# Kernel tuning notes

Hardware: AMD Instinct MI355X
Metric: run time of the kernel (lower is better)

## Reference

```python
import jax, jax.numpy as jnp
import numpy as np

N, E, S = 20000, 160000, 3        # nodes, edges, message-passing steps
L, NODE_D, EDGE_D, OUT = 128, 12, 7, 3
LN_EPS = 1e-5


def _mlp(x, W0, b0, W1, b1, W2, b2):
    # Linear -> ReLU -> Linear -> ReLU -> Linear (widths: in->L->L->out)
    h = jax.nn.relu(x @ W0 + b0)
    h = jax.nn.relu(h @ W1 + b1)
    return h @ W2 + b2


def _ln(h, g, b):
    mu = jnp.mean(h, axis=-1, keepdims=True)
    var = jnp.mean((h - mu) ** 2, axis=-1, keepdims=True)
    return (h - mu) * jax.lax.rsqrt(var + LN_EPS) * g + b


def setup_inputs() -> dict:
    ks = iter(jax.random.split(jax.random.key(0), 64))
    w = lambda *s: jax.random.normal(next(ks), s, jnp.float32) * 0.05
    z = lambda *s: jnp.zeros(s, jnp.float32)
    o = lambda *s: jnp.ones(s, jnp.float32)
    inp = {
        'node_x': jax.random.normal(next(ks), (N, NODE_D), jnp.float32),
        'edge_x': jax.random.normal(next(ks), (E, EDGE_D), jnp.float32),
        'enc_n_W0': w(NODE_D, L), 'enc_n_b0': z(L), 'enc_n_W1': w(L, L), 'enc_n_b1': z(L),
        'enc_n_W2': w(L, L), 'enc_n_b2': z(L), 'enc_n_g': o(L), 'enc_n_be': z(L),
        'enc_e_W0': w(EDGE_D, L), 'enc_e_b0': z(L), 'enc_e_W1': w(L, L), 'enc_e_b1': z(L),
        'enc_e_W2': w(L, L), 'enc_e_b2': z(L), 'enc_e_g': o(L), 'enc_e_be': z(L),
        'gnb_e_W0': w(S, 3 * L, L), 'gnb_e_b0': z(S, L), 'gnb_e_W1': w(S, L, L), 'gnb_e_b1': z(S, L),
        'gnb_e_W2': w(S, L, L), 'gnb_e_b2': z(S, L), 'gnb_e_g': o(S, L), 'gnb_e_be': z(S, L),
        'gnb_n_W0': w(S, 2 * L, L), 'gnb_n_b0': z(S, L), 'gnb_n_W1': w(S, L, L), 'gnb_n_b1': z(S, L),
        'gnb_n_W2': w(S, L, L), 'gnb_n_b2': z(S, L), 'gnb_n_g': o(S, L), 'gnb_n_be': z(S, L),
        'dec_W0': w(L, L), 'dec_b0': z(L), 'dec_W1': w(L, L), 'dec_b1': z(L),
        'dec_W2': w(L, OUT), 'dec_b2': z(OUT),
        'senders': jax.random.randint(next(ks), (E,), 0, N, jnp.int32),
        'receivers': jax.random.randint(next(ks), (E,), 0, N, jnp.int32),
    }
    return inp


def reference(node_x, edge_x,
              enc_n_W0, enc_n_b0, enc_n_W1, enc_n_b1, enc_n_W2, enc_n_b2, enc_n_g, enc_n_be,
              enc_e_W0, enc_e_b0, enc_e_W1, enc_e_b1, enc_e_W2, enc_e_b2, enc_e_g, enc_e_be,
              gnb_e_W0, gnb_e_b0, gnb_e_W1, gnb_e_b1, gnb_e_W2, gnb_e_b2, gnb_e_g, gnb_e_be,
              gnb_n_W0, gnb_n_b0, gnb_n_W1, gnb_n_b1, gnb_n_W2, gnb_n_b2, gnb_n_g, gnb_n_be,
              dec_W0, dec_b0, dec_W1, dec_b1, dec_W2, dec_b2,
              senders, receivers):
    num_nodes = node_x.shape[0]
    # Encoder: MLP + LayerNorm on nodes and edges
    nf = _ln(_mlp(node_x, enc_n_W0, enc_n_b0, enc_n_W1, enc_n_b1, enc_n_W2, enc_n_b2), enc_n_g, enc_n_be)
    ef = _ln(_mlp(edge_x, enc_e_W0, enc_e_b0, enc_e_W1, enc_e_b1, enc_e_W2, enc_e_b2), enc_e_g, enc_e_be)

    def step(carry, p):
        nf, ef = carry
        (eW0, eb0, eW1, eb1, eW2, eb2, eg, ebe,
         nW0, nb0, nW1, nb1, nW2, nb2, ng, nbe) = p
        # gather sender/receiver node features -> concat with edge features -> edge MLP
        cat_e = jnp.concatenate([nf[senders], nf[receivers], ef], axis=-1)  # [E, 3L]
        new_ef = _ln(_mlp(cat_e, eW0, eb0, eW1, eb1, eW2, eb2), eg, ebe)
        # scatter-sum updated edge features to receiver nodes
        agg = jax.ops.segment_sum(new_ef, receivers, num_segments=num_nodes)  # [N, L]
        new_nf = _ln(_mlp(jnp.concatenate([nf, agg], axis=-1), nW0, nb0, nW1, nb1, nW2, nb2), ng, nbe)
        # residual connections on both nodes and edges
        return (nf + new_nf, ef + new_ef), None

    step_params = (gnb_e_W0, gnb_e_b0, gnb_e_W1, gnb_e_b1, gnb_e_W2, gnb_e_b2, gnb_e_g, gnb_e_be,
                   gnb_n_W0, gnb_n_b0, gnb_n_W1, gnb_n_b1, gnb_n_W2, gnb_n_b2, gnb_n_g, gnb_n_be)
    (nf, ef), _ = jax.lax.scan(step, (nf, ef), step_params)

    # Decoder: MLP without LayerNorm
    return _mlp(nf, dec_W0, dec_b0, dec_W1, dec_b1, dec_W2, dec_b2)
```

## Files before the change

### kernel.cpp

```cpp
#include <hip/hip_runtime.h>
#include <hip/hip_bf16.h>

#define NN 20000
#define EE 160000

typedef __attribute__((ext_vector_type(8))) short bf16x8;
typedef __attribute__((ext_vector_type(4))) float f32x4;

__device__ __forceinline__ unsigned short f2bf(float f) {
    unsigned int u = __float_as_uint(f);
    u += 0x7FFFu + ((u >> 16) & 1);
    return (unsigned short)(u >> 16);
}
__device__ __forceinline__ float bf2f(short s) {
    return __uint_as_float(((unsigned int)(unsigned short)s) << 16);
}
__device__ __forceinline__ bf16x8 pack8(float4 a, float4 b) {
    bf16x8 r;
    r[0] = (short)f2bf(a.x); r[1] = (short)f2bf(a.y);
    r[2] = (short)f2bf(a.z); r[3] = (short)f2bf(a.w);
    r[4] = (short)f2bf(b.x); r[5] = (short)f2bf(b.y);
    r[6] = (short)f2bf(b.z); r[7] = (short)f2bf(b.w);
    return r;
}
// ... 20 lines not shown

__device__ __forceinline__ void mfma_sweep64(f32x4 (&acc)[2][8], bf16x8 a0, bf16x8 a1,
                                             const short* sWb, int colOff, int lm)
{
#pragma unroll
    for (int ct = 0; ct < 8; ++ct) {
        bf16x8 b = *(const bf16x8*)(sWb + (ct * 16 + lm) * SW64 + colOff);
        acc[0][ct] = __builtin_amdgcn_mfma_f32_16x16x32_bf16(a0, b, acc[0][ct], 0, 0, 0);
        acc[1][ct] = __builtin_amdgcn_mfma_f32_16x16x32_bf16(a1, b, acc[1][ct], 0, 0, 0);
    }
}

__device__ __forceinline__ void mfma_sweepNS(f32x4 (&acc)[4], bf16x8 a,
                                             const short* sWb, int ch, int colOff, int lm)
{
#pragma unroll
    for (int i = 0; i < 4; ++i) {
        int ct = ch * 4 + i;
        bf16x8 b = *(const bf16x8*)(sWb + (ct * 16 + lm) * SW64 + colOff);
        acc[i] = __builtin_amdgcn_mfma_f32_16x16x32_bf16(a, b, acc[i], 0, 0, 0);
    }
}

template<int NT>
struct WStage { bf16x8 v[512 / NT]; };

template<int NT>
__device__ __forceinline__ void wload(WStage<NT>& ws, const short* __restrict__ Wt,
                                      int Kpad, int k0, int tid)
{
#pragma unroll
    for (int j = 0; j < 256 / NT; ++j) {
        int i = tid + j * NT;
        int r = i >> 1, h = i & 1;
        const short* src = Wt + (size_t)r * Kpad + k0 + h * 16;
        ws.v[2 * j]     = *(const bf16x8*)src;
        ws.v[2 * j + 1] = *(const bf16x8*)(src + 8);
    }
}
template<int NT>
__device__ __forceinline__ void wstore(const WStage<NT>& ws, short* __restrict__ sW, int tid)
{
#pragma unroll
    for (int j = 0; j < 256 / NT; ++j) {
        int i = tid + j * NT;
        int r = i >> 1, h = i & 1;
        short* dst = sW + r * SW_STRIDE + h * 16;
        *(bf16x8*)dst       = ws.v[2 * j];
        *(bf16x8*)(dst + 8) = ws.v[2 * j + 1];
    }
}

struct WStage64 { bf16x8 v[4]; };
__device__ __forceinline__ void wload64(WStage64& ws, const short* __restrict__ Wt,
                                        int Kpad, int k0, int tid)
{
#pragma unroll
    for (int j = 0; j < 4; ++j) {
        int i = tid + j * 256;
        int r = i >> 3, h = i & 7;
        ws.v[j] = *(const bf16x8*)(Wt + (size_t)r * Kpad + k0 + h * 8);
    }
}
__device__ __forceinline__ void wstore64(const WStage64& ws, short* __restrict__ sW, int tid)
{
#pragma unroll
    for (int j = 0; j < 4; ++j) {
        int i = tid + j * 256;
        int r = i >> 3, h = i & 7;
        *(bf16x8*)(sW + r * SW64 + h * 8) = ws.v[j];
    }
}

// ... 35 lines not shown
            sH[(g16 + lq * 4 + reg) * SH_STRIDE + ct * 16 + lm] = (short)f2bf(v);
        }
    }
}

__device__ __forceinline__ void park64(const f32x4 (&acc)[2][8], const float* __restrict__ bias,
                                       short* __restrict__ sH, int w32, int lm, int lq)
{
#pragma unroll
    for (int ct = 0; ct < 8; ++ct) {
        float bb = bias[ct * 16 + lm];
#pragma unroll
        for (int rt = 0; rt < 2; ++rt) {
            int rbase = w32 + rt * 16 + lq * 4;
#pragma unroll
            for (int reg = 0; reg < 4; ++reg) {
                float v = fmaxf(acc[rt][ct][reg] + bb, 0.f);
                sH[(rbase + reg) * SH64 + ct * 16 + lm] = (short)f2bf(v);
            }
        }
    }
}

struct Frag {
    bf16x8 a0, a1;
    float4 f0, f1, f2, f3;
    int isF;
};

template<int MODE>
__device__ __forceinline__ void load_frag(Frag& fr, int c,
    const short* __restrict__ nfb, const float* __restrict__ aggf,
    int r0m, int r1m, const short* sH, int w32, int lm, int lq)
{
    int kq = lq * 8;
    fr.isF = 0;
    if (MODE == 0) {
        fr.a0 = *(const bf16x8*)&sH[(w32 + lm) * SH_STRIDE + c * 32 + kq];
        fr.a1 = *(const bf16x8*)&sH[(w32 + 16 + lm) * SH_STRIDE + c * 32 + kq];
    } else if (MODE == 2) {
        int seg = c >> 2, kb = (c & 3) * 32 + kq;
        if (seg == 0) {
            fr.a0 = *(const bf16x8*)(nfb + (size_t)r0m * 128 + kb);
            fr.a1 = *(const bf16x8*)(nfb + (size_t)r1m * 128 + kb);
        } else {
            const float* p0 = aggf + (size_t)r0m * 128 + kb;
            const float* p1 = aggf + (size_t)r1m * 128 + kb;
            fr.f0 = *(const float4*)p0; fr.f1 = *(const float4*)(p0 + 4);
            fr.f2 = *(const float4*)p1; fr.f3 = *(const float4*)(p1 + 4);
            fr.isF = 1;
        }
    } else {
        int kb = c * 32 + kq;
        fr.a0 = *(const bf16x8*)(nfb + (size_t)r0m * 128 + kb);
        fr.a1 = *(const bf16x8*)(nfb + (size_t)r1m * 128 + kb);
    }
}

template<int MODE>
__device__ __forceinline__ void load_fragNS(Frag& fr, int c,
    const short* __restrict__ nfb, const float* __restrict__ aggf, int r0m, int lq)
{
    fr.isF = 0;
    if (MODE == 2 && c >= 2) {
        const float* p = aggf + (size_t)r0m * 128 + (c - 2) * 64 + lq * 8;
        fr.f0 = *(const float4*)p;        fr.f1 = *(const float4*)(p + 4);
        fr.f2 = *(const float4*)(p + 32); fr.f3 = *(const float4*)(p + 36);
        fr.isF = 1;
    } else {
        const short* p = nfb + (size_t)r0m * 128 + c * 64 + lq * 8;
        fr.a0 = *(const bf16x8*)p;
        fr.a1 = *(const bf16x8*)(p + 32);
    }
}

struct Frag64 { bf16x8 a[4]; };

__device__ __forceinline__ void load_frag64(Frag64& fr, int c,
    const short* __restrict__ nfb, const short* __restrict__ efHi,
    int iS0, int iS1, int iR0, int iR1, size_t eO0, size_t eO1, int lq)
{
    int kb = (c & 1) * 64 + lq * 8;
    int seg = c >> 1;
    const short *base0, *base1;
    if (seg == 0)      { base0 = nfb + (size_t)iS0 * 128; base1 = nfb + (size_t)iS1 * 128; }
    else if (seg == 1) { base0 = nfb + (size_t)iR0 * 128; base1 = nfb + (size_t)iR1 * 128; }
    else               { base0 = efHi + eO0;              base1 = efHi + eO1; }
// ... 143 lines not shown
            }
        }
        if (rcv != curRcv) {
            if (curRcv >= 0) {
#pragma unroll
                for (int ct = 0; ct < 8; ++ct)
                    atomicAdd(aggOut + (size_t)curRcv * 128 + ct * 16 + lm, run[ct]);
            }
            curRcv = rcv;
#pragma unroll
            for (int ct = 0; ct < 8; ++ct) run[ct] = o[ct];
        } else {
#pragma unroll
            for (int ct = 0; ct < 8; ++ct) run[ct] += o[ct];
        }
    }
    if (curRcv >= 0) {
#pragma unroll
        for (int ct = 0; ct < 8; ++ct)
            atomicAdd(aggOut + (size_t)curRcv * 128 + ct * 16 + lm, run[ct]);
    }
}

template<int NW, int MODE, int PAIR>
__global__ __launch_bounds__(NW * 64) void gnn_mlp(
    const short* __restrict__ Wt0,
    const short* __restrict__ Wt1, const short* __restrict__ Wt2,
    const float* __restrict__ b0, const float* __restrict__ b1, const float* __restrict__ b2,
    const float* __restrict__ g, const float* __restrict__ be,
    const float* __restrict__ A0f, int K0,
    const short* __restrict__ nfb,
    const float* __restrict__ aggf,
    const int* __restrict__ eList,
    float* __restrict__ outF, short* __restrict__ outB,
    float* __restrict__ aggOut,
    float* __restrict__ decOut,
    int M, int resid)
{
    constexpr int KP0 = (MODE == 2) ? 256 : (MODE == 3) ? 128 : 32;
    constexpr int nC0 = KP0 / 32;
    __shared__ short sH[NW * 32 * SH_STRIDE];
    __shared__ short sW[128 * SW_STRIDE];
    const int tid = threadIdx.x;
    const int lane = tid & 63;
    const int w = tid >> 6;
    const int lm = lane & 15;
    const int lq = lane >> 4;
    const int w32 = w * 32;
    const int m0 = blockIdx.x * (NW * 32);
    constexpr int NT = NW * 64;

    f32x4 acc[2][8];
    zero_acc(acc);

    if (MODE == 0) {
#pragma unroll
        for (int i = 0; i < 16; ++i) {
            int flat = lane + i * 64;
            int r = flat >> 5, k = flat & 31;
            int row = m0 + w32 + r;
            float v = 0.f;
            if (k < K0 && row < M) {
                int src = eList ? eList[row] : row;
                v = A0f[(size_t)src * K0 + k];
            }
            sH[(w32 + r) * SH_STRIDE + k] = (short)f2bf(v);
        }
    }
    const int r0m = min(m0 + w32 + lm, M - 1);
    const int r1m = min(m0 + w32 + 16 + lm, M - 1);

    {
        WStage<NT> ws, wsn;
        Frag cur, nx1, nx2;
        wload<NT>(ws, Wt0, KP0, 0, tid);
        load_frag<MODE>(cur, 0, nfb, aggf, r0m, r1m, sH, w32, lm, lq);
        if (nC0 > 1)
            load_frag<MODE>(nx1, 1, nfb, aggf, r0m, r1m, sH, w32, lm, lq);
#pragma unroll
        for (int c = 0; c < nC0; ++c) {
            if (c + 1 < nC0)
                wload<NT>(wsn, Wt0, KP0, (c + 1) * 32, tid);
            if (c + 2 < nC0)
                load_frag<MODE>(nx2, c + 2, nfb, aggf, r0m, r1m, sH, w32, lm, lq);
            bar_lgkm();
            wstore<NT>(ws, sW, tid);
            bar_lgkm();
            bf16x8 u0, u1;
            if (cur.isF) { u0 = pack8(cur.f0, cur.f1); u1 = pack8(cur.f2, cur.f3); }
            else         { u0 = cur.a0;               u1 = cur.a1; }
            mfma_sweep_lds(acc, u0, u1, sW, lm, lq);
            ws = wsn; cur = nx1; nx1 = nx2;
        }
    }
    bar_lgkm();
    park(acc, b0, sH, w32, lm, lq);

    zero_acc(acc);
    {
        WStage<NT> ws, wsn;
        wload<NT>(ws, Wt1, 128, 0, tid);
#pragma unroll
        for (int c = 0; c < 4; ++c) {
            if (c + 1 < 4) wload<NT>(wsn, Wt1, 128, (c + 1) * 32, tid);
            bf16x8 a0 = *(const bf16x8*)&sH[(w32 + lm) * SH_STRIDE + c * 32 + lq * 8];
            bf16x8 a1 = *(const bf16x8*)&sH[(w32 + 16 + lm) * SH_STRIDE + c * 32 + lq * 8];
            bar_lgkm();
            wstore<NT>(ws, sW, tid);
            bar_lgkm();
            mfma_sweep_lds(acc, a0, a1, sW, lm, lq);
            ws = wsn;
        }
    }
    bar_lgkm();
    park(acc, b1, sH, w32, lm, lq);

    zero_acc(acc);
    {
        WStage<NT> ws, wsn;
        wload<NT>(ws, Wt2, 128, 0, tid);
#pragma unroll
        for (int c = 0; c < 4; ++c) {
            if (c + 1 < 4) wload<NT>(wsn, Wt2, 128, (c + 1) * 32, tid);
            bf16x8 a0 = *(const bf16x8*)&sH[(w32 + lm) * SH_STRIDE + c * 32 + lq * 8];
            bf16x8 a1 = *(const bf16x8*)&sH[(w32 + 16 + lm) * SH_STRIDE + c * 32 + lq * 8];
            bar_lgkm();
            wstore<NT>(ws, sW, tid);
            bar_lgkm();
            mfma_sweep_lds(acc, a0, a1, sW, lm, lq);
            ws = wsn;
        }
    }

    float g_[8], be_[8], b2_[8];
#pragma unroll
    for (int ct = 0; ct < 8; ++ct) {
        g_[ct] = g[ct * 16 + lm]; be_[ct] = be[ct * 16 + lm]; b2_[ct] = b2[ct * 16 + lm];
    }
#pragma unroll
    for (int rt = 0; rt < 2; ++rt) {
#pragma unroll
        for (int reg = 0; reg < 4; ++reg) {
            int row = m0 + w32 + rt * 16 + lq * 4 + reg;
            float v[8];
            float s = 0.f;
#pragma unroll
            for (int ct = 0; ct < 8; ++ct) { v[ct] = acc[rt][ct][reg] + b2_[ct]; s += v[ct]; }
            s += __shfl_xor(s, 1); s += __shfl_xor(s, 2);
            s += __shfl_xor(s, 4); s += __shfl_xor(s, 8);
            float mu = s * (1.f / 128.f);
            float q = 0.f;
#pragma unroll
            for (int ct = 0; ct < 8; ++ct) { v[ct] -= mu; q += v[ct] * v[ct]; }
            q += __shfl_xor(q, 1); q += __shfl_xor(q, 2);
            q += __shfl_xor(q, 4); q += __shfl_xor(q, 8);
            float rs = rsqrtf(q * (1.f / 128.f) + 1e-5f);
            if (row < M) {
#pragma unroll
                for (int ct = 0; ct < 8; ++ct) {
                    float o = v[ct] * rs * g_[ct] + be_[ct];
                    size_t gi = (size_t)row * 128 + ct * 16 + lm;
                    if (PAIR) {
                        outB[gi] = (short)f2bf(o);
                    } else {
                        if (resid) {
                            float ns = outF[gi] + o;
                            outF[gi] = ns;
                            if (outB) outB[gi] = (short)f2bf(ns);
                        } else {
                            outF[gi] = o;
                            if (outB) outB[gi] = (short)f2bf(o);
                        }
                    }
                }
            }
        }
    }
}

template<int MODE>
__global__ __launch_bounds__(256) void gnn_mlpNS(
    const short* __restrict__ Wt0,
    const short* __restrict__ Wt1, const short* __restrict__ Wt2,
    const float* __restrict__ b0, const float* __restrict__ b1, const float* __restrict__ b2,
    const float* __restrict__ g, const float* __restrict__ be,
    const float* __restrict__ A0f, int K0,
    const short* __restrict__ nfb,
    const float* __restrict__ aggf,
    float* __restrict__ outF, short* __restrict__ outB,
    float* __restrict__ aggOut,
    float* __restrict__ decOut,
    int M, int resid)
{
    __shared__ short sH[32 * SH_STRIDE];
    __shared__ short sW[128 * SW64];
    __shared__ float sX[2][32];
    __shared__ float sY[2][32];
    const int tid = threadIdx.x;
    const int lane = tid & 63;
    const int w = tid >> 6;
    const int gidx = w >> 1;
    const int ch = w & 1;
    const int lm = lane & 15;
    const int lq = lane >> 4;
    const int g16 = gidx * 16;
    const int m0 = blockIdx.x * 32;
    const int r0m = min(m0 + g16 + lm, M - 1);

    f32x4 acc[4];
#pragma unroll
    for (int i = 0; i < 4; ++i) acc[i] = (f32x4)(0.f);

    if (MODE == 0) {
#pragma unroll
        for (int i = 0; i < 4; ++i) {
            int flat = tid + i * 256;
            int r = flat >> 5, k = flat & 31;
            int row = m0 + r;
            float v = (k < K0 && row < M) ? A0f[(size_t)row * K0 + k] : 0.f;
            sH[r * SH_STRIDE + k] = (short)f2bf(v);
        }
        {
            const short* src = Wt0 + (size_t)(tid >> 1) * 32 + (tid & 1) * 16;
            bf16x8 w0 = *(const bf16x8*)src;
            bf16x8 w1 = *(const bf16x8*)(src + 8);
            bar_lgkm();
            short* dst = sW + (tid >> 1) * SW64 + (tid & 1) * 16;
            *(bf16x8*)dst       = w0;
            *(bf16x8*)(dst + 8) = w1;
            bar_lgkm();
        }
        bf16x8 a0 = *(const bf16x8*)&sH[(g16 + lm) * SH_STRIDE + lq * 8];
        mfma_sweepNS(acc, a0, sW, ch, lq * 8, lm);
    } else {
        constexpr int KP0 = (MODE == 2) ? 256 : 128;
        constexpr int nC0 = KP0 / 64;
        WStage64 ws, wsn;
        Frag cur, nxt;
        wload64(ws, Wt0, KP0, 0, tid);
        load_fragNS<MODE>(cur, 0, nfb, aggf, r0m, lq);
#pragma unroll
        for (int c = 0; c < nC0; ++c) {
            if (c + 1 < nC0) {
                wload64(wsn, Wt0, KP0, (c + 1) * 64, tid);
                load_fragNS<MODE>(nxt, c + 1, nfb, aggf, r0m, lq);
            }
            bar_lgkm();
            wstore64(ws, sW, tid);
            bar_lgkm();
            bf16x8 u0, u1;
            if (cur.isF) { u0 = pack8(cur.f0, cur.f1); u1 = pack8(cur.f2, cur.f3); }
            else         { u0 = cur.a0;                u1 = cur.a1; }
            mfma_sweepNS(acc, u0, sW, ch, lq * 8, lm);
            mfma_sweepNS(acc, u1, sW, ch, 32 + lq * 8, lm);
            ws = wsn; cur = nxt;
        }
    }
    bar_lgkm();
    parkNS(acc, b0, sH, g16, ch, lm, lq);
    bar_lgkm();

    if (MODE == 2 && aggOut) {
#pragma unroll
        for (int i = 0; i < 4; ++i) {
            int idx = tid + i * 256;
            int r = idx >> 5, c4 = idx & 31;
            int row = m0 + r;
            if (row < M)
// ... 3 lines not shown

#pragma unroll
    for (int i = 0; i < 4; ++i) acc[i] = (f32x4)(0.f);
    {
        WStage64 ws, wsn;
        wload64(ws, Wt1, 128, 0, tid);
#pragma unroll
        for (int c = 0; c < 2; ++c) {
            if (c == 0) wload64(wsn, Wt1, 128, 64, tid);
            bf16x8 a0 = *(const bf16x8*)&sH[(g16 + lm) * SH_STRIDE + c * 64 + lq * 8];
            bf16x8 a1 = *(const bf16x8*)&sH[(g16 + lm) * SH_STRIDE + c * 64 + 32 + lq * 8];
            bar_lgkm();
            wstore64(ws, sW, tid);
            bar_lgkm();
            mfma_sweepNS(acc, a0, sW, ch, lq * 8, lm);
            mfma_sweepNS(acc, a1, sW, ch, 32 + lq * 8, lm);
            ws = wsn;
        }
    }
    bar_lgkm();
    parkNS(acc, b1, sH, g16, ch, lm, lq);
    bar_lgkm();

    if (MODE == 3) {
        if (tid < 96) {
            int r = tid / 3, o = tid - r * 3;
            int row = m0 + r;
            if (row < M) {
                float s = b2[o];
#pragma unroll
                for (int kk = 0; kk < 16; ++kk) {
                    bf16x8 h8 = *(const bf16x8*)&sH[r * SH_STRIDE + kk * 8];
#pragma unroll
                    for (int j = 0; j < 8; ++j)
                        s += bf2f(h8[j]) * A0f[(kk * 8 + j) * 3 + o];
                }
                decOut[(size_t)row * 3 + o] = s;
            }
        }
        return;
    }

#pragma unroll
    for (int i = 0; i < 4; ++i) acc[i] = (f32x4)(0.f);
    {
        WStage64 ws, wsn;
        wload64(ws, Wt2, 128, 0, tid);
#pragma unroll
        for (int c = 0; c < 2; ++c) {
            if (c == 0) wload64(wsn, Wt2, 128, 64, tid);
            bf16x8 a0 = *(const bf16x8*)&sH[(g16 + lm) * SH_STRIDE + c * 64 + lq * 8];
            bf16x8 a1 = *(const bf16x8*)&sH[(g16 + lm) * SH_STRIDE + c * 64 + 32 + lq * 8];
            bar_lgkm();
            wstore64(ws, sW, tid);
            bar_lgkm();
            mfma_sweepNS(acc, a0, sW, ch, lq * 8, lm);
            mfma_sweepNS(acc, a1, sW, ch, 32 + lq * 8, lm);
            ws = wsn;
        }
    }

    float g_[4], be_[4], b2_[4];
#pragma unroll
    for (int i = 0; i < 4; ++i) {
        int ct = ch * 4 + i;
        g_[i] = g[ct * 16 + lm]; be_[i] = be[ct * 16 + lm]; b2_[i] = b2[ct * 16 + lm];
    }
    float v[4][4], mu[4], rs_[4];
#pragma unroll
    for (int reg = 0; reg < 4; ++reg) {
        float s = 0.f;
#pragma unroll
        for (int i = 0; i < 4; ++i) { v[i][reg] = acc[i][reg] + b2_[i]; s += v[i][reg]; }
        s += __shfl_xor(s, 1); s += __shfl_xor(s, 2);
        s += __shfl_xor(s, 4); s += __shfl_xor(s, 8);
        if (lm == 0) sX[ch][g16 + lq * 4 + reg] = s;
    }
    bar_lgkm();
#pragma unroll
    for (int reg = 0; reg < 4; ++reg)
        mu[reg] = (sX[0][g16 + lq * 4 + reg] + sX[1][g16 + lq * 4 + reg]) * (1.f / 128.f);
#pragma unroll
    for (int reg = 0; reg < 4; ++reg) {
        float q = 0.f;
#pragma unroll
        for (int i = 0; i < 4; ++i) { v[i][reg] -= mu[reg]; q += v[i][reg] * v[i][reg]; }
        q += __shfl_xor(q, 1); q += __shfl_xor(q, 2);
        q += __shfl_xor(q, 4); q += __shfl_xor(q, 8);
        if (lm == 0) sY[ch][g16 + lq * 4 + reg] = q;
    }
    bar_lgkm();
#pragma unroll
    for (int reg = 0; reg < 4; ++reg)
        rs_[reg] = rsqrtf((sY[0][g16 + lq * 4 + reg] + sY[1][g16 + lq * 4 + reg]) * (1.f / 128.f) + 1e-5f);
#pragma unroll
    for (int reg = 0; reg < 4; ++reg) {
        int row = m0 + g16 + lq * 4 + reg;
        if (row < M) {
#pragma unroll
            for (int i = 0; i < 4; ++i) {
                float o = v[i][reg] * rs_[reg] * g_[i] + be_[i];
                size_t gi = (size_t)row * 128 + (size_t)(ch * 4 + i) * 16 + lm;
                if (resid) {
                    float ns = outF[gi] + o;
                    outF[gi] = ns;
                    if (outB) outB[gi] = (short)f2bf(ns);
                } else {
                    outF[gi] = o;
                    if (outB) outB[gi] = (short)f2bf(o);
                }
            }
        }
    }
}

__global__ void zero_i(int* __restrict__ p, int n)
{
    int i = blockIdx.x * 256 + threadIdx.x;
    if (i < n) p[i] = 0;
}
__global__ void csr_count(const int* __restrict__ recv, int* __restrict__ cnt, int E)
{
    int i = blockIdx.x * 256 + threadIdx.x;
    if (i < E) atomicAdd(&cnt[recv[i]], 1);
}
__global__ __launch_bounds__(256) void csr_scan(const int* __restrict__ cnt,
                                                int* __restrict__ cursor, int N)
{
    __shared__ int ssum[257];
    const int tid = threadIdx.x;
    const int per = (N + 255) / 256;
    const int lo = tid * per, hi = min(lo + per, N);
    int s = 0;
    for (int i = lo; i < hi; ++i) s += cnt[i];
    ssum[tid] = s;
    __syncthreads();
// ... 119 lines not shown
        o_ge0[s] = add(gnb_e_W0 + (size_t)s * 384 * 128, 384, 384);
        o_ge1[s] = add(gnb_e_W1 + (size_t)s * 128 * 128, 128, 128);
        o_ge2[s] = add(gnb_e_W2 + (size_t)s * 128 * 128, 128, 128);
        o_gn0[s] = add(gnb_n_W0 + (size_t)s * 256 * 128, 256, 256);
        o_gn1[s] = add(gnb_n_W1 + (size_t)s * 128 * 128, 128, 128);
        o_gn2[s] = add(gnb_n_W2 + (size_t)s * 128 * 128, 128, 128);
    }
    o_dec[0] = add(dec_W0, 128, 128);
    o_dec[1] = add(dec_W1, 128, 128);

    wt_prep_kernel<<<dim3(192, 26), 256, 0, stream>>>(tbl, wt);

    if (useSorted) {
        zero_i<<<dim3((N + 255) / 256), 256, 0, stream>>>(cnt, N);
        csr_count<<<dim3((E + 255) / 256), 256, 0, stream>>>(receivers, cnt, E);
        csr_scan<<<dim3(1), 256, 0, stream>>>(cnt, cursor, N);
        csr_fill<<<dim3((E + 255) / 256), 256, 0, stream>>>(receivers, cursor, eList, E);
    }
    zero_kernel<<<dim3((N * 32 + 255) / 256), 256, 0, stream>>>((float4*)agg, (long)N * 32);

    const dim3 gE(E / 128);
    const dim3 gNS(N / 32);

    gnn_mlpNS<0><<<gNS, 256, 0, stream>>>(wt + o_encn[0], wt + o_encn[1], wt + o_encn[2],
        enc_n_b0, enc_n_b1, enc_n_b2, enc_n_g, enc_n_be,
        node_x, 12, nullptr, nullptr,
        nf, nfbf, nullptr, nullptr, N, 0);
    gnn_mlp<4, 0, 1><<<gE, 256, 0, stream>>>(wt + o_ence[0], wt + o_ence[1], wt + o_ence[2],
        enc_e_b0, enc_e_b1, enc_e_b2, enc_e_g, enc_e_be,
        edge_x, 7, nullptr, nullptr, eL,
        nullptr, efHi, nullptr, nullptr, E, 0);

    for (int s = 0; s < 3; ++s) {
        const float* eb0 = gnb_e_b0 + (size_t)s * 128;
        const float* eb1 = gnb_e_b1 + (size_t)s * 128;
        const float* eb2 = gnb_e_b2 + (size_t)s * 128;
        const float* eg  = gnb_e_g  + (size_t)s * 128;
        const float* ebe = gnb_e_be + (size_t)s * 128;
        const float* nb0 = gnb_n_b0 + (size_t)s * 128;
        const float* nb1 = gnb_n_b1 + (size_t)s * 128;
        const float* nb2 = gnb_n_b2 + (size_t)s * 128;
        const float* ng  = gnb_n_g  + (size_t)s * 128;
        const float* nbe = gnb_n_be + (size_t)s * 128;

        if (s < 2) {
            gnn_edge64<1><<<gE, 256, 0, stream>>>(wt + o_ge0[s], wt + o_ge1[s], wt + o_ge2[s],
                eb0, eb1, eb2, eg, ebe,
                nfbf, efHi, eL, senders, receivers, agg);
        } else {
            gnn_edge64<0><<<gE, 256, 0, stream>>>(wt + o_ge0[s], wt + o_ge1[s], wt + o_ge2[s],
                eb0, eb1, eb2, eg, ebe,
                nfbf, efHi, eL, senders, receivers, agg);
        }
        gnn_mlpNS<2><<<gNS, 256, 0, stream>>>(wt + o_gn0[s], wt + o_gn1[s], wt + o_gn2[s],
            nb0, nb1, nb2, ng, nbe,
            nullptr, 0, nfbf, agg,
            nf, nfbf, agg, nullptr, N, 1);
    }

    gnn_mlpNS<3><<<gNS, 256, 0, stream>>>(wt + o_dec[0], wt + o_dec[1], nullptr,
        dec_b0, dec_b1, dec_b2, nullptr, nullptr,
        dec_W2, 0, nfbf, nullptr,
        nullptr, nullptr, nullptr, out, N, 0);
}
```

Measured before the change: 539.6 us.

## Merge node and edge encoders into one launch and fuse decoder into final node step

The node encoder and edge encoder now run as one kernel, with the block index choosing which body to execute, so the two independent encoders share the GPU and one launch is saved. The last message-passing node MLP now runs the decoder MLP on the updated node features while they are still in shared memory. This skips writing and re-reading the final node state and removes the separate decoder launch. The generic templated MLP kernel is specialised into smaller bodies, and the fused kernels reserve a larger shared-memory footprint, which may lower occupancy.

After: 584.3 us. 1.08x slower.

```diff
diff --git a/kernel.cpp b/kernel.cpp
--- a/kernel.cpp
+++ b/kernel.cpp
@@ -66,33 +66,21 @@
     }
 }
 
-template<int NT>
-struct WStage { bf16x8 v[512 / NT]; };
-
-template<int NT>
-__device__ __forceinline__ void wload(WStage<NT>& ws, const short* __restrict__ Wt,
-                                      int Kpad, int k0, int tid)
-{
-#pragma unroll
-    for (int j = 0; j < 256 / NT; ++j) {
-        int i = tid + j * NT;
-        int r = i >> 1, h = i & 1;
-        const short* src = Wt + (size_t)r * Kpad + k0 + h * 16;
-        ws.v[2 * j]     = *(const bf16x8*)src;
-        ws.v[2 * j + 1] = *(const bf16x8*)(src + 8);
-    }
-}
-template<int NT>
-__device__ __forceinline__ void wstore(const WStage<NT>& ws, short* __restrict__ sW, int tid)
-{
-#pragma unroll
-    for (int j = 0; j < 256 / NT; ++j) {
-        int i = tid + j * NT;
-        int r = i >> 1, h = i & 1;
-        short* dst = sW + r * SW_STRIDE + h * 16;
-        *(bf16x8*)dst       = ws.v[2 * j];
-        *(bf16x8*)(dst + 8) = ws.v[2 * j + 1];
-    }
+struct WStageE { bf16x8 v[2]; };
+__device__ __forceinline__ void wloadE(WStageE& ws, const short* __restrict__ Wt,
+                                       int Kpad, int k0, int tid)
+{
+    int r = tid >> 1, h = tid & 1;
+    const short* src = Wt + (size_t)r * Kpad + k0 + h * 16;
+    ws.v[0] = *(const bf16x8*)src;
+    ws.v[1] = *(const bf16x8*)(src + 8);
+}
+__device__ __forceinline__ void wstoreE(const WStageE& ws, short* __restrict__ sW, int tid)
+{
+    int r = tid >> 1, h = tid & 1;
+    short* dst = sW + r * SW_STRIDE + h * 16;
+    *(bf16x8*)dst       = ws.v[0];
+    *(bf16x8*)(dst + 8) = ws.v[1];
 }
 
 struct WStage64 { bf16x8 v[4]; };
@@ -174,47 +162,16 @@
     }
 }
 
-struct Frag {
+struct FragNS {
     bf16x8 a0, a1;
     float4 f0, f1, f2, f3;
     int isF;
 };
-
-template<int MODE>
-__device__ __forceinline__ void load_frag(Frag& fr, int c,
-    const short* __restrict__ nfb, const float* __restrict__ aggf,
-    int r0m, int r1m, const short* sH, int w32, int lm, int lq)
-{
-    int kq = lq * 8;
+__device__ __forceinline__ void load_fragNS(FragNS& fr, int c,
+    const short* __restrict__ nfb, const float* __restrict__ aggf, int r0m, int lq)
+{
     fr.isF = 0;
-    if (MODE == 0) {
-        fr.a0 = *(const bf16x8*)&sH[(w32 + lm) * SH_STRIDE + c * 32 + kq];
-        fr.a1 = *(const bf16x8*)&sH[(w32 + 16 + lm) * SH_STRIDE + c * 32 + kq];
-    } else if (MODE == 2) {
-        int seg = c >> 2, kb = (c & 3) * 32 + kq;
-        if (seg == 0) {
-            fr.a0 = *(const bf16x8*)(nfb + (size_t)r0m * 128 + kb);
-            fr.a1 = *(const bf16x8*)(nfb + (size_t)r1m * 128 + kb);
-        } else {
-            const float* p0 = aggf + (size_t)r0m * 128 + kb;
-            const float* p1 = aggf + (size_t)r1m * 128 + kb;
-            fr.f0 = *(const float4*)p0; fr.f1 = *(const float4*)(p0 + 4);
-            fr.f2 = *(const float4*)p1; fr.f3 = *(const float4*)(p1 + 4);
-            fr.isF = 1;
-        }
-    } else {
-        int kb = c * 32 + kq;
-        fr.a0 = *(const bf16x8*)(nfb + (size_t)r0m * 128 + kb);
-        fr.a1 = *(const bf16x8*)(nfb + (size_t)r1m * 128 + kb);
-    }
-}
-
-template<int MODE>
-__device__ __forceinline__ void load_fragNS(Frag& fr, int c,
-    const short* __restrict__ nfb, const float* __restrict__ aggf, int r0m, int lq)
-{
-    fr.isF = 0;
-    if (MODE == 2 && c >= 2) {
+    if (c >= 2) {
         const float* p = aggf + (size_t)r0m * 128 + (c - 2) * 64 + lq * 8;
         fr.f0 = *(const float4*)p;        fr.f1 = *(const float4*)(p + 4);
         fr.f2 = *(const float4*)(p + 32); fr.f3 = *(const float4*)(p + 36);
@@ -404,180 +361,25 @@
     }
 }
 
-template<int NW, int MODE, int PAIR>
-__global__ __launch_bounds__(NW * 64) void gnn_mlp(
-    const short* __restrict__ Wt0,
-    const short* __restrict__ Wt1, const short* __restrict__ Wt2,
+template<int MODE>
+__device__ __forceinline__ void ns_body(char* smem, int bid,
+    const short* __restrict__ Wt0, const short* __restrict__ Wt1, const short* __restrict__ Wt2,
     const float* __restrict__ b0, const float* __restrict__ b1, const float* __restrict__ b2,
     const float* __restrict__ g, const float* __restrict__ be,
     const float* __restrict__ A0f, int K0,
-    const short* __restrict__ nfb,
-    const float* __restrict__ aggf,
-    const int* __restrict__ eList,
+    const short* __restrict__ nfb, const float* __restrict__ aggf,
     float* __restrict__ outF, short* __restrict__ outB,
-    float* __restrict__ aggOut,
-    float* __restrict__ decOut,
+    float* __restrict__ aggOut, float* __restrict__ decOut,
+    const short* __restrict__ Wd0, const short* __restrict__ Wd1,
+    const float* __restrict__ dW2f,
+    const float* __restrict__ db0, const float* __restrict__ db1,
+    const float* __restrict__ db2,
     int M, int resid)
 {
-    constexpr int KP0 = (MODE == 2) ? 256 : (MODE == 3) ? 128 : 32;
-    constexpr int nC0 = KP0 / 32;
-    __shared__ short sH[NW * 32 * SH_STRIDE];
-    __shared__ short sW[128 * SW_STRIDE];
-    const int tid = threadIdx.x;
-    const int lane = tid & 63;
-    const int w = tid >> 6;
-    const int lm = lane & 15;
-    const int lq = lane >> 4;
-    const int w32 = w * 32;
-    const int m0 = blockIdx.x * (NW * 32);
-    constexpr int NT = NW * 64;
-
-    f32x4 acc[2][8];
-    zero_acc(acc);
-
-    if (MODE == 0) {
-#pragma unroll
-        for (int i = 0; i < 16; ++i) {
-            int flat = lane + i * 64;
-            int r = flat >> 5, k = flat & 31;
-            int row = m0 + w32 + r;
-            float v = 0.f;
-            if (k < K0 && row < M) {
-                int src = eList ? eList[row] : row;
-                v = A0f[(size_t)src * K0 + k];
-            }
-            sH[(w32 + r) * SH_STRIDE + k] = (short)f2bf(v);
-        }
-    }
-    const int r0m = min(m0 + w32 + lm, M - 1);
-    const int r1m = min(m0 + w32 + 16 + lm, M - 1);
-
-    {
-        WStage<NT> ws, wsn;
-        Frag cur, nx1, nx2;
-        wload<NT>(ws, Wt0, KP0, 0, tid);
-        load_frag<MODE>(cur, 0, nfb, aggf, r0m, r1m, sH, w32, lm, lq);
-        if (nC0 > 1)
-            load_frag<MODE>(nx1, 1, nfb, aggf, r0m, r1m, sH, w32, lm, lq);
-#pragma unroll
-        for (int c = 0; c < nC0; ++c) {
-            if (c + 1 < nC0)
-                wload<NT>(wsn, Wt0, KP0, (c + 1) * 32, tid);
-            if (c + 2 < nC0)
-                load_frag<MODE>(nx2, c + 2, nfb, aggf, r0m, r1m, sH, w32, lm, lq);
-            bar_lgkm();
-            wstore<NT>(ws, sW, tid);
-            bar_lgkm();
-            bf16x8 u0, u1;
-            if (cur.isF) { u0 = pack8(cur.f0, cur.f1); u1 = pack8(cur.f2, cur.f3); }
-            else         { u0 = cur.a0;               u1 = cur.a1; }
-            mfma_sweep_lds(acc, u0, u1, sW, lm, lq);
-            ws = wsn; cur = nx1; nx1 = nx2;
-        }
-    }
-    bar_lgkm();
-    park(acc, b0, sH, w32, lm, lq);
-
-    zero_acc(acc);
-    {
-        WStage<NT> ws, wsn;
-        wload<NT>(ws, Wt1, 128, 0, tid);
-#pragma unroll
-        for (int c = 0; c < 4; ++c) {
-            if (c + 1 < 4) wload<NT>(wsn, Wt1, 128, (c + 1) * 32, tid);
-            bf16x8 a0 = *(const bf16x8*)&sH[(w32 + lm) * SH_STRIDE + c * 32 + lq * 8];
-            bf16x8 a1 = *(const bf16x8*)&sH[(w32 + 16 + lm) * SH_STRIDE + c * 32 + lq * 8];
-            bar_lgkm();
-            wstore<NT>(ws, sW, tid);
-            bar_lgkm();
-            mfma_sweep_lds(acc, a0, a1, sW, lm, lq);
-            ws = wsn;
-        }
-    }
-    bar_lgkm();
-    park(acc, b1, sH, w32, lm, lq);
-
-    zero_acc(acc);
-    {
-        WStage<NT> ws, wsn;
-        wload<NT>(ws, Wt2, 128, 0, tid);
-#pragma unroll
-        for (int c = 0; c < 4; ++c) {
-            if (c + 1 < 4) wload<NT>(wsn, Wt2, 128, (c + 1) * 32, tid);
-            bf16x8 a0 = *(const bf16x8*)&sH[(w32 + lm) * SH_STRIDE + c * 32 + lq * 8];
-            bf16x8 a1 = *(const bf16x8*)&sH[(w32 + 16 + lm) * SH_STRIDE + c * 32 + lq * 8];
-            bar_lgkm();
-            wstore<NT>(ws, sW, tid);
-            bar_lgkm();
-            mfma_sweep_lds(acc, a0, a1, sW, lm, lq);
-            ws = wsn;
-        }
-    }
-
-    float g_[8], be_[8], b2_[8];
-#pragma unroll
-    for (int ct = 0; ct < 8; ++ct) {
-        g_[ct] = g[ct * 16 + lm]; be_[ct] = be[ct * 16 + lm]; b2_[ct] = b2[ct * 16 + lm];
-    }
-#pragma unroll
-    for (int rt = 0; rt < 2; ++rt) {
-#pragma unroll
-        for (int reg = 0; reg < 4; ++reg) {
-            int row = m0 + w32 + rt * 16 + lq * 4 + reg;
-            float v[8];
-            float s = 0.f;
-#pragma unroll
-            for (int ct = 0; ct < 8; ++ct) { v[ct] = acc[rt][ct][reg] + b2_[ct]; s += v[ct]; }
-            s += __shfl_xor(s, 1); s += __shfl_xor(s, 2);
-            s += __shfl_xor(s, 4); s += __shfl_xor(s, 8);
-            float mu = s * (1.f / 128.f);
-            float q = 0.f;
-#pragma unroll
-            for (int ct = 0; ct < 8; ++ct) { v[ct] -= mu; q += v[ct] * v[ct]; }
-            q += __shfl_xor(q, 1); q += __shfl_xor(q, 2);
-            q += __shfl_xor(q, 4); q += __shfl_xor(q, 8);
-            float rs = rsqrtf(q * (1.f / 128.f) + 1e-5f);
-            if (row < M) {
-#pragma unroll
-                for (int ct = 0; ct < 8; ++ct) {
-                    float o = v[ct] * rs * g_[ct] + be_[ct];
-                    size_t gi = (size_t)row * 128 + ct * 16 + lm;
-                    if (PAIR) {
-                        outB[gi] = (short)f2bf(o);
-                    } else {
-                        if (resid) {
-                            float ns = outF[gi] + o;
-                            outF[gi] = ns;
-                            if (outB) outB[gi] = (short)f2bf(ns);
-                        } else {
-                            outF[gi] = o;
-                            if (outB) outB[gi] = (short)f2bf(o);
-                        }
-                    }
-                }
-            }
-        }
-    }
-}
-
-template<int MODE>
-__global__ __launch_bounds__(256) void gnn_mlpNS(
-    const short* __restrict__ Wt0,
-    const short* __restrict__ Wt1, const short* __restrict__ Wt2,
-    const float* __restrict__ b0, const float* __restrict__ b1, const float* __restrict__ b2,
-    const float* __restrict__ g, const float* __restrict__ be,
-    const float* __restrict__ A0f, int K0,
-    const short* __restrict__ nfb,
-    const float* __restrict__ aggf,
-    float* __restrict__ outF, short* __restrict__ outB,
-    float* __restrict__ aggOut,
-    float* __restrict__ decOut,
-    int M, int resid)
-{
-    __shared__ short sH[32 * SH_STRIDE];
-    __shared__ short sW[128 * SW64];
-    __shared__ float sX[2][32];
-    __shared__ float sY[2][32];
+    short* sH = (short*)smem;
+    short* sW = (short*)(smem + 8704);
+    float* sX = (float*)(smem + 8704 + 18432);
+    float* sY = sX + 64;
     const int tid = threadIdx.x;
     const int lane = tid & 63;
     const int w = tid >> 6;
@@ -586,7 +388,7 @@
     const int lm = lane & 15;
     const int lq = lane >> 4;
     const int g16 = gidx * 16;
-    const int m0 = blockIdx.x * 32;
+    const int m0 = bid * 32;
     const int r0m = min(m0 + g16 + lm, M - 1);
 
     f32x4 acc[4];
@@ -615,17 +417,15 @@
         bf16x8 a0 = *(const bf16x8*)&sH[(g16 + lm) * SH_STRIDE + lq * 8];
         mfma_sweepNS(acc, a0, sW, ch, lq * 8, lm);
     } else {
-        constexpr int KP0 = (MODE == 2) ? 256 : 128;
-        constexpr int nC0 = KP0 / 64;
         WStage64 ws, wsn;
-        Frag cur, nxt;
-        wload64(ws, Wt0, KP0, 0, tid);
-        load_fragNS<MODE>(cur, 0, nfb, aggf, r0m, lq);
-#pragma unroll
-        for (int c = 0; c < nC0; ++c) {
-            if (c + 1 < nC0) {
-                wload64(wsn, Wt0, KP0, (c + 1) * 64, tid);
-                load_fragNS<MODE>(nxt, c + 1, nfb, aggf, r0m, lq);
+        FragNS cur, nxt;
+        wload64(ws, Wt0, 256, 0, tid);
+        load_fragNS(cur, 0, nfb, aggf, r0m, lq);
+#pragma unroll
+        for (int c = 0; c < 4; ++c) {
+            if (c + 1 < 4) {
+                wload64(wsn, Wt0, 256, (c + 1) * 64, tid);
+                load_fragNS(nxt, c + 1, nfb, aggf, r0m, lq);
             }
             bar_lgkm();
             wstore64(ws, sW, tid);
@@ -675,18 +475,128 @@
     parkNS(acc, b1, sH, g16, ch, lm, lq);
     bar_lgkm();
 
-    if (MODE == 3) {
+#pragma unroll
+    for (int i = 0; i < 4; ++i) acc[i] = (f32x4)(0.f);
+    {
+        WStage64 ws, wsn;
+        wload64(ws, Wt2, 128, 0, tid);
+#pragma unroll
+        for (int c = 0; c < 2; ++c) {
+            if (c == 0) wload64(wsn, Wt2, 128, 64, tid);
+            bf16x8 a0 = *(const bf16x8*)&sH[(g16 + lm) * SH_STRIDE + c * 64 + lq * 8];
+            bf16x8 a1 = *(const bf16x8*)&sH[(g16 + lm) * SH_STRIDE + c * 64 + 32 + lq * 8];
+            bar_lgkm();
+            wstore64(ws, sW, tid);
+            bar_lgkm();
+            mfma_sweepNS(acc, a0, sW, ch, lq * 8, lm);
+            mfma_sweepNS(acc, a1, sW, ch, 32 + lq * 8, lm);
+            ws = wsn;
+        }
+    }
+
+    float g_[4], be_[4], b2_[4];
+#pragma unroll
+    for (int i = 0; i < 4; ++i) {
+        int ct = ch * 4 + i;
+        g_[i] = g[ct * 16 + lm]; be_[i] = be[ct * 16 + lm]; b2_[i] = b2[ct * 16 + lm];
+    }
+    float v[4][4], mu[4], rs_[4];
+#pragma unroll
+    for (int reg = 0; reg < 4; ++reg) {
+        float s = 0.f;
+#pragma unroll
+        for (int i = 0; i < 4; ++i) { v[i][reg] = acc[i][reg] + b2_[i]; s += v[i][reg]; }
+        s += __shfl_xor(s, 1); s += __shfl_xor(s, 2);
+        s += __shfl_xor(s, 4); s += __shfl_xor(s, 8);
+        if (lm == 0) sX[ch * 32 + g16 + lq * 4 + reg] = s;
+    }
+    bar_lgkm();
+#pragma unroll
+    for (int reg = 0; reg < 4; ++reg)
+        mu[reg] = (sX[g16 + lq * 4 + reg] + sX[32 + g16 + lq * 4 + reg]) * (1.f / 128.f);
+#pragma unroll
+    for (int reg = 0; reg < 4; ++reg) {
+        float q = 0.f;
+#pragma unroll
+        for (int i = 0; i < 4; ++i) { v[i][reg] -= mu[reg]; q += v[i][reg] * v[i][reg]; }
+        q += __shfl_xor(q, 1); q += __shfl_xor(q, 2);
+        q += __shfl_xor(q, 4); q += __shfl_xor(q, 8);
+        if (lm == 0) sY[ch * 32 + g16 + lq * 4 + reg] = q;
+    }
+    bar_lgkm();
+#pragma unroll
+    for (int reg = 0; reg < 4; ++reg)
+        rs_[reg] = rsqrtf((sY[g16 + lq * 4 + reg] + sY[32 + g16 + lq * 4 + reg]) * (1.f / 128.f) + 1e-5f);
+
+    if (MODE == 4) {
+#pragma unroll
+        for (int reg = 0; reg < 4; ++reg) {
+            int row = m0 + g16 + lq * 4 + reg;
+#pragma unroll
+            for (int i = 0; i < 4; ++i) {
+                float o = v[i][reg] * rs_[reg] * g_[i] + be_[i];
+                size_t gi = (size_t)row * 128 + (size_t)(ch * 4 + i) * 16 + lm;
+                float ns = outF[gi] + o;
+                sH[(g16 + lq * 4 + reg) * SH_STRIDE + (ch * 4 + i) * 16 + lm] = (short)f2bf(ns);
+            }
+        }
+        bar_lgkm();
+
+#pragma unroll
+        for (int i = 0; i < 4; ++i) acc[i] = (f32x4)(0.f);
+        {
+            WStage64 ws, wsn;
+            wload64(ws, Wd0, 128, 0, tid);
+#pragma unroll
+            for (int c = 0; c < 2; ++c) {
+                if (c == 0) wload64(wsn, Wd0, 128, 64, tid);
+                bf16x8 a0 = *(const bf16x8*)&sH[(g16 + lm) * SH_STRIDE + c * 64 + lq * 8];
+                bf16x8 a1 = *(const bf16x8*)&sH[(g16 + lm) * SH_STRIDE + c * 64 + 32 + lq * 8];
+                bar_lgkm();
+                wstore64(ws, sW, tid);
+                bar_lgkm();
+                mfma_sweepNS(acc, a0, sW, ch, lq * 8, lm);
+                mfma_sweepNS(acc, a1, sW, ch, 32 + lq * 8, lm);
+                ws = wsn;
+            }
+        }
+        bar_lgkm();
+        parkNS(acc, db0, sH, g16, ch, lm, lq);
+        bar_lgkm();
+
+#pragma unroll
+        for (int i = 0; i < 4; ++i) acc[i] = (f32x4)(0.f);
+        {
+            WStage64 ws, wsn;
+            wload64(ws, Wd1, 128, 0, tid);
+#pragma unroll
+            for (int c = 0; c < 2; ++c) {
+                if (c == 0) wload64(wsn, Wd1, 128, 64, tid);
+                bf16x8 a0 = *(const bf16x8*)&sH[(g16 + lm) * SH_STRIDE + c * 64 + lq * 8];
+                bf16x8 a1 = *(const bf16x8*)&sH[(g16 + lm) * SH_STRIDE + c * 64 + 32 + lq * 8];
+                bar_lgkm();
+                wstore64(ws, sW, tid);
+                bar_lgkm();
+                mfma_sweepNS(acc, a0, sW, ch, lq * 8, lm);
+                mfma_sweepNS(acc, a1, sW, ch, 32 + lq * 8, lm);
+                ws = wsn;
+            }
+        }
+        bar_lgkm();
+        parkNS(acc, db1, sH, g16, ch, lm, lq);
+        bar_lgkm();
+
         if (tid < 96) {
             int r = tid / 3, o = tid - r * 3;
             int row = m0 + r;
             if (row < M) {
-                float s = b2[o];
+                float s = db2[o];
 #pragma unroll
                 for (int kk = 0; kk < 16; ++kk) {
                     bf16x8 h8 = *(const bf16x8*)&sH[r * SH_STRIDE + kk * 8];
 #pragma unroll
                     for (int j = 0; j < 8; ++j)
-                        s += bf2f(h8[j]) * A0f[(kk * 8 + j) * 3 + o];
+                        s += bf2f(h8[j]) * dW2f[(kk * 8 + j) * 3 + o];
                 }
                 decOut[(size_t)row * 3 + o] = s;
             }
@@ -694,58 +604,6 @@
         return;
     }
 
-#pragma unroll
-    for (int i = 0; i < 4; ++i) acc[i] = (f32x4)(0.f);
-    {
-        WStage64 ws, wsn;
-        wload64(ws, Wt2, 128, 0, tid);
-#pragma unroll
-        for (int c = 0; c < 2; ++c) {
-            if (c == 0) wload64(wsn, Wt2, 128, 64, tid);
-            bf16x8 a0 = *(const bf16x8*)&sH[(g16 + lm) * SH_STRIDE + c * 64 + lq * 8];
-            bf16x8 a1 = *(const bf16x8*)&sH[(g16 + lm) * SH_STRIDE + c * 64 + 32 + lq * 8];
-            bar_lgkm();
-            wstore64(ws, sW, tid);
-            bar_lgkm();
-            mfma_sweepNS(acc, a0, sW, ch, lq * 8, lm);
-            mfma_sweepNS(acc, a1, sW, ch, 32 + lq * 8, lm);
-            ws = wsn;
-        }
-    }
-
-    float g_[4], be_[4], b2_[4];
-#pragma unroll
-    for (int i = 0; i < 4; ++i) {
-        int ct = ch * 4 + i;
-        g_[i] = g[ct * 16 + lm]; be_[i] = be[ct * 16 + lm]; b2_[i] = b2[ct * 16 + lm];
-    }
-    float v[4][4], mu[4], rs_[4];
-#pragma unroll
-    for (int reg = 0; reg < 4; ++reg) {
-        float s = 0.f;
-#pragma unroll
-        for (int i = 0; i < 4; ++i) { v[i][reg] = acc[i][reg] + b2_[i]; s += v[i][reg]; }
-        s += __shfl_xor(s, 1); s += __shfl_xor(s, 2);
-        s += __shfl_xor(s, 4); s += __shfl_xor(s, 8);
-        if (lm == 0) sX[ch][g16 + lq * 4 + reg] = s;
-    }
-    bar_lgkm();
-#pragma unroll
-    for (int reg = 0; reg < 4; ++reg)
-        mu[reg] = (sX[0][g16 + lq * 4 + reg] + sX[1][g16 + lq * 4 + reg]) * (1.f / 128.f);
-#pragma unroll
-    for (int reg = 0; reg < 4; ++reg) {
-        float q = 0.f;
-#pragma unroll
-        for (int i = 0; i < 4; ++i) { v[i][reg] -= mu[reg]; q += v[i][reg] * v[i][reg]; }
-        q += __shfl_xor(q, 1); q += __shfl_xor(q, 2);
-        q += __shfl_xor(q, 4); q += __shfl_xor(q, 8);
-        if (lm == 0) sY[ch][g16 + lq * 4 + reg] = q;
-    }
-    bar_lgkm();
-#pragma unroll
-    for (int reg = 0; reg < 4; ++reg)
-        rs_[reg] = rsqrtf((sY[0][g16 + lq * 4 + reg] + sY[1][g16 + lq * 4 + reg]) * (1.f / 128.f) + 1e-5f);
 #pragma unroll
     for (int reg = 0; reg < 4; ++reg) {
         int row = m0 + g16 + lq * 4 + reg;
@@ -765,6 +623,176 @@
             }
         }
     }
+}
+
+__device__ __forceinline__ void ence_body(char* smem, int bid,
+    const short* __restrict__ Wt0, const short* __restrict__ Wt1, const short* __restrict__ Wt2,
+    const float* __restrict__ b0, const float* __restrict__ b1, const float* __restrict__ b2,
+    const float* __restrict__ g, const float* __restrict__ be,
+    const float* __restrict__ A0f, int K0,
+    const int* __restrict__ eList,
+    short* __restrict__ outB, int M)
+{
+    short* sH = (short*)smem;
+    short* sW = (short*)(smem + 34816);
+    const int tid = threadIdx.x;
+    const int lane = tid & 63;
+    const int w = tid >> 6;
+    const int lm = lane & 15;
+    const int lq = lane >> 4;
+    const int w32 = w * 32;
+    const int m0 = bid * 128;
+
+    f32x4 acc[2][8];
+    zero_acc(acc);
+
+#pragma unroll
+    for (int i = 0; i < 16; ++i) {
+        int flat = lane + i * 64;
+        int r = flat >> 5, k = flat & 31;
+        int row = m0 + w32 + r;
+        float v = 0.f;
+        if (k < K0 && row < M) {
+            int src = eList ? eList[row] : row;
+            v = A0f[(size_t)src * K0 + k];
+        }
+        sH[(w32 + r) * SH_STRIDE + k] = (short)f2bf(v);
+    }
+    {
+        WStageE ws;
+        wloadE(ws, Wt0, 32, 0, tid);
+        bf16x8 a0 = *(const bf16x8*)&sH[(w32 + lm) * SH_STRIDE + lq * 8];
+        bf16x8 a1 = *(const bf16x8*)&sH[(w32 + 16 + lm) * SH_STRIDE + lq * 8];
+        bar_lgkm();
+        wstoreE(ws, sW, tid);
+        bar_lgkm();
+        mfma_sweep_lds(acc, a0, a1, sW, lm, lq);
+    }
+    bar_lgkm();
+    park(acc, b0, sH, w32, lm, lq);
+
+    zero_acc(acc);
+    {
+        WStageE ws, wsn;
+        wloadE(ws, Wt1, 128, 0, tid);
+#pragma unroll
+        for (int c = 0; c < 4; ++c) {
+            if (c + 1 < 4) wloadE(wsn, Wt1, 128, (c + 1) * 32, tid);
+            bf16x8 a0 = *(const bf16x8*)&sH[(w32 + lm) * SH_STRIDE + c * 32 + lq * 8];
+            bf16x8 a1 = *(const bf16x8*)&sH[(w32 + 16 + lm) * SH_STRIDE + c * 32 + lq * 8];
+            bar_lgkm();
+            wstoreE(ws, sW, tid);
+            bar_lgkm();
+            mfma_sweep_lds(acc, a0, a1, sW, lm, lq);
+            ws = wsn;
+        }
+    }
+    bar_lgkm();
+    park(acc, b1, sH, w32, lm, lq);
+
+    zero_acc(acc);
+    {
+        WStageE ws, wsn;
+        wloadE(ws, Wt2, 128, 0, tid);
+#pragma unroll
+        for (int c = 0; c < 4; ++c) {
+            if (c + 1 < 4) wloadE(wsn, Wt2, 128, (c + 1) * 32, tid);
+            bf16x8 a0 = *(const bf16x8*)&sH[(w32 + lm) * SH_STRIDE + c * 32 + lq * 8];
+            bf16x8 a1 = *(const bf16x8*)&sH[(w32 + 16 + lm) * SH_STRIDE + c * 32 + lq * 8];
+            bar_lgkm();
+            wstoreE(ws, sW, tid);
+            bar_lgkm();
+            mfma_sweep_lds(acc, a0, a1, sW, lm, lq);
+            ws = wsn;
+        }
+    }
+
+    float g_[8], be_[8], b2_[8];
+#pragma unroll
+    for (int ct = 0; ct < 8; ++ct) {
+        g_[ct] = g[ct * 16 + lm]; be_[ct] = be[ct * 16 + lm]; b2_[ct] = b2[ct * 16 + lm];
+    }
+#pragma unroll
+    for (int rt = 0; rt < 2; ++rt) {
+#pragma unroll
+        for (int reg = 0; reg < 4; ++reg) {
+            int row = m0 + w32 + rt * 16 + lq * 4 + reg;
+            float vv[8];
+            float s = 0.f;
+#pragma unroll
+            for (int ct = 0; ct < 8; ++ct) { vv[ct] = acc[rt][ct][reg] + b2_[ct]; s += vv[ct]; }
+            s += __shfl_xor(s, 1); s += __shfl_xor(s, 2);
+            s += __shfl_xor(s, 4); s += __shfl_xor(s, 8);
+            float mu = s * (1.f / 128.f);
+            float q = 0.f;
+#pragma unroll
+            for (int ct = 0; ct < 8; ++ct) { vv[ct] -= mu; q += vv[ct] * vv[ct]; }
+            q += __shfl_xor(q, 1); q += __shfl_xor(q, 2);
+            q += __shfl_xor(q, 4); q += __shfl_xor(q, 8);
+            float rs = rsqrtf(q * (1.f / 128.f) + 1e-5f);
+            if (row < M) {
+#pragma unroll
+                for (int ct = 0; ct < 8; ++ct) {
+                    float o = vv[ct] * rs * g_[ct] + be_[ct];
+                    outB[(size_t)row * 128 + ct * 16 + lm] = (short)f2bf(o);
+                }
+            }
+        }
+    }
+}
+
+__global__ __launch_bounds__(256) void gnn_enc_both(
+    const short* __restrict__ nW0, const short* __restrict__ nW1, const short* __restrict__ nW2,
+    const float* __restrict__ nb0, const float* __restrict__ nb1, const float* __restrict__ nb2,
+    const float* __restrict__ ng, const float* __restrict__ nbe,
+    const float* __restrict__ node_x, int nK0,
+    float* __restrict__ nf, short* __restrict__ nfbf, int NM,
+    const short* __restrict__ eW0, const short* __restrict__ eW1, const short* __restrict__ eW2,
+    const float* __restrict__ eb0, const float* __restrict__ eb1, const float* __restrict__ eb2,
+    const float* __restrict__ eg, const float* __restrict__ ebe,
+    const float* __restrict__ edge_x, int eK0,
+    const int* __restrict__ eList, short* __restrict__ efB, int EM)
+{
+    __shared__ __align__(16) char smem[49152];
+    if ((int)blockIdx.x < NN / 32) {
+        ns_body<0>(smem, blockIdx.x, nW0, nW1, nW2, nb0, nb1, nb2, ng, nbe,
+                   node_x, nK0, nullptr, nullptr, nf, nfbf, nullptr, nullptr,
+                   nullptr, nullptr, nullptr, nullptr, nullptr, nullptr, NM, 0);
+    } else {
+        ence_body(smem, blockIdx.x - NN / 32, eW0, eW1, eW2, eb0, eb1, eb2, eg, ebe,
+                  edge_x, eK0, eList, efB, EM);
+    }
+}
+
+__global__ __launch_bounds__(256) void gnn_nodeNS(
+    const short* __restrict__ Wt0, const short* __restrict__ Wt1, const short* __restrict__ Wt2,
+    const float* __restrict__ b0, const float* __restrict__ b1, const float* __restrict__ b2,
+    const float* __restrict__ g, const float* __restrict__ be,
+    const short* __restrict__ nfb, const float* __restrict__ aggf,
+    float* __restrict__ outF, short* __restrict__ outB, float* __restrict__ aggOut, int M)
+{
+    __shared__ __align__(16) char smem[27648];
+    ns_body<2>(smem, blockIdx.x, Wt0, Wt1, Wt2, b0, b1, b2, g, be,
+               nullptr, 0, nfb, aggf, outF, outB, aggOut, nullptr,
+               nullptr, nullptr, nullptr, nullptr, nullptr, nullptr, M, 1);
+}
+
+__global__ __launch_bounds__(256) void gnn_node_dec(
+    const short* __restrict__ Wt0, const short* __restrict__ Wt1, const short* __restrict__ Wt2,
+    const float* __restrict__ b0, const float* __restrict__ b1, const float* __restrict__ b2,
+    const float* __restrict__ g, const float* __restrict__ be,
+    const short* __restrict__ nfb, const float* __restrict__ aggf,
+    float* __restrict__ nfF,
+    const short* __restrict__ Wd0, const short* __restrict__ Wd1,
+    const float* __restrict__ dW2f,
+    const float* __restrict__ db0, const float* __restrict__ db1,
+    const float* __restrict__ db2,
+    float* __restrict__ decOut, int M)
+{
+    __shared__ __align__(16) char smem[27648];
+    ns_body<4>(smem, blockIdx.x, Wt0, Wt1, Wt2, b0, b1, b2, g, be,
+               nullptr, 0, nfb, aggf, nfF, nullptr, nullptr, decOut,
+               Wd0, Wd1, dW2f, db0, db1, db2, M, 1);
 }
 
 __global__ void zero_i(int* __restrict__ p, int n)
@@ -930,14 +958,13 @@
     const dim3 gE(E / 128);
     const dim3 gNS(N / 32);
 
-    gnn_mlpNS<0><<<gNS, 256, 0, stream>>>(wt + o_encn[0], wt + o_encn[1], wt + o_encn[2],
+    gnn_enc_both<<<dim3(N / 32 + E / 128), 256, 0, stream>>>(
+        wt + o_encn[0], wt + o_encn[1], wt + o_encn[2],
         enc_n_b0, enc_n_b1, enc_n_b2, enc_n_g, enc_n_be,
-        node_x, 12, nullptr, nullptr,
-        nf, nfbf, nullptr, nullptr, N, 0);
-    gnn_mlp<4, 0, 1><<<gE, 256, 0, stream>>>(wt + o_ence[0], wt + o_ence[1], wt + o_ence[2],
+        node_x, 12, nf, nfbf, N,
+        wt + o_ence[0], wt + o_ence[1], wt + o_ence[2],
         enc_e_b0, enc_e_b1, enc_e_b2, enc_e_g, enc_e_be,
-        edge_x, 7, nullptr, nullptr, eL,
-        nullptr, efHi, nullptr, nullptr, E, 0);
+        edge_x, 7, eL, efHi, E);
 
     for (int s = 0; s < 3; ++s) {
         const float* eb0 = gnb_e_b0 + (size_t)s * 128;
@@ -955,19 +982,19 @@
             gnn_edge64<1><<<gE, 256, 0, stream>>>(wt + o_ge0[s], wt + o_ge1[s], wt + o_ge2[s],
                 eb0, eb1, eb2, eg, ebe,
                 nfbf, efHi, eL, senders, receivers, agg);
+            gnn_nodeNS<<<gNS, 256, 0, stream>>>(wt + o_gn0[s], wt + o_gn1[s], wt + o_gn2[s],
+                nb0, nb1, nb2, ng, nbe,
+                nfbf, agg, nf, nfbf, agg, N);
         } else {
             gnn_edge64<0><<<gE, 256, 0, stream>>>(wt + o_ge0[s], wt + o_ge1[s], wt + o_ge2[s],
                 eb0, eb1, eb2, eg, ebe,
                 nfbf, efHi, eL, senders, receivers, agg);
-        }
-        gnn_mlpNS<2><<<gNS, 256, 0, stream>>>(wt + o_gn0[s], wt + o_gn1[s], wt + o_gn2[s],
-            nb0, nb1, nb2, ng, nbe,
-            nullptr, 0, nfbf, agg,
-            nf, nfbf, agg, nullptr, N, 1);
-    }
-
-    gnn_mlpNS<3><<<gNS, 256, 0, stream>>>(wt + o_dec[0], wt + o_dec[1], nullptr,
-        dec_b0, dec_b1, dec_b2, nullptr, nullptr,
-        dec_W2, 0, nfbf, nullptr,
-        nullptr, nullptr, nullptr, out, N, 0);
-}
+            gnn_node_dec<<<gNS, 256, 0, stream>>>(wt + o_gn0[s], wt + o_gn1[s], wt + o_gn2[s],
+                nb0, nb1, nb2, ng, nbe,
+                nfbf, agg, nf,
+                wt + o_dec[0], wt + o_dec[1], dec_W2,
+                dec_b0, dec_b1, dec_b2,
+                out, N);
+        }
+    }
+}
```
